# Performance work log

Hardware: AMD Instinct MI355X
Metric: run time of the kernel (lower is better)

Reference implementation:

```python
import jax, jax.numpy as jnp
import numpy as np

N_FIELDS = 8
N_NODES = 100000
N_EDGES = 6400000


def setup_inputs() -> dict:
    key = jax.random.key(0)
    k1, k2, k3, k4, k5 = jax.random.split(key, 5)
    q = jax.random.normal(k1, (N_FIELDS, N_NODES), dtype=jnp.float32)
    edges = jax.random.normal(k2, (N_EDGES, 1), dtype=jnp.float32)
    senders = jax.random.randint(k3, (N_EDGES,), 0, N_NODES, dtype=jnp.int32)
    receivers = jax.random.randint(k4, (N_EDGES,), 0, N_NODES, dtype=jnp.int32)
    dt = jax.random.uniform(k5, (1,), dtype=jnp.float32)
    # learned parameters, initialized exactly as in DeltaQGNN.__init__
    w_self = jnp.linspace(0.05, 0.09, N_FIELDS)
    w_msg = jnp.linspace(0.02, 0.04, N_FIELDS)
    w_edge = jnp.linspace(0.01, 0.03, N_FIELDS)
    b = jnp.linspace(0.005, 0.008, N_FIELDS)
    return {"q": q, "edges": edges, "senders": senders, "receivers": receivers,
            "dt": dt, "w_self": w_self, "w_msg": w_msg, "w_edge": w_edge, "b": b}


def reference(q, edges, senders, receivers, dt, w_self, w_msg, w_edge, b):
    # q: [F, N], edges: [E, 1], senders/receivers: [E], dt: [1]
    n_nodes = q.shape[1]
    edge_scalar = edges[:, 0]                                    # [E]
    # gather sender values for all fields at once: [F, E]
    msg_in = q[:, senders] + w_edge[:, None] * edge_scalar[None, :]
    # scatter-add to receivers per field: [F, N]
    msg = jax.vmap(lambda m: jax.ops.segment_sum(m, receivers, num_segments=n_nodes))(msg_in)
    rhs = w_self[:, None] * q + w_msg[:, None] * msg + b[:, None]
    return dt * rhs                                              # [F, N]
```

## Files before the change

### kernel.cpp

```cpp
#include <hip/hip_runtime.h>

#define NF 8
#define BSHIFT 8
#define BNODES 256
#define MAXNB 512
#define TPB 256
#define TPR 512
#define TPBF 512
#define CHUNKF 3072
#define KPE 6
#define NBLKF 1024
#define CAPB 17408
#define SPLIT 8
#define CAP 24
#define IDXSTR 26
#define LSLICE 2560

__global__ void k_transpose(const float* __restrict__ q, float* __restrict__ qT,
                            float* __restrict__ govf, unsigned* __restrict__ gcur,
                            int n_nodes, int nb) {
    int n = blockIdx.x * blockDim.x + threadIdx.x;
    if (n < nb) gcur[n] = 0u;
    if (n >= n_nodes) return;
    float4 a, b;
    a.x = q[0 * n_nodes + n]; a.y = q[1 * n_nodes + n];
    a.z = q[2 * n_nodes + n]; a.w = q[3 * n_nodes + n];
    b.x = q[4 * n_nodes + n]; b.y = q[5 * n_nodes + n];
    b.z = q[6 * n_nodes + n]; b.w = q[7 * n_nodes + n];
    float4* dst = reinterpret_cast<float4*>(qT + (size_t)n * NF);
    dst[0] = a; dst[1] = b;
    float* o = govf + (size_t)n * 9;
#pragma unroll
    for (int k = 0; k < 9; ++k) o[k] = 0.f;
}

__global__ __launch_bounds__(TPBF) void k_scatter_fused(
        const float* __restrict__ edges, const int* __restrict__ senders,
        const int* __restrict__ receivers, int n_edges, int nb, int tiles,
        unsigned* __restrict__ gcur, const float* __restrict__ qT,
        float* __restrict__ govf, uint2* __restrict__ rec) {
    __shared__ uint2 lrec[CHUNKF];
    __shared__ unsigned short lbkt[CHUNKF];
    __shared__ unsigned hist[MAXNB];
    __shared__ unsigned lbase[MAXNB];
    __shared__ unsigned gbase[MAXNB];

    for (int t = blockIdx.x; t < tiles; t += gridDim.x) {
        int start = t * CHUNKF;
        int end = min(start + CHUNKF, n_edges);
        int n = end - start;

        for (int i = threadIdx.x; i < nb; i += TPBF) hist[i] = 0u;
        __syncthreads();

        unsigned rcx[KPE], rcy[KPE], meta[KPE];
#pragma unroll
        for (int k = 0; k < KPE; ++k) {
            int i = (int)threadIdx.x + k * TPBF;
            meta[k] = 0xFFFFFFFFu;
            if (i < n) {
                int e = start + i;
                int s = senders[e];
                int r = receivers[e];
                float ev = edges[e];
                unsigned bkt = (unsigned)r >> BSHIFT;
                unsigned p = atomicAdd(&hist[bkt], 1u);
                rcx[k] = ((unsigned)(r & (BNODES - 1)) << 17) | (unsigned)s;
                rcy[k] = __float_as_uint(ev);
                meta[k] = (p << 9) | bkt;
            }
        }
        __syncthreads();

        if (threadIdx.x < (unsigned)nb)
            gbase[threadIdx.x] = atomicAdd(&gcur[threadIdx.x], hist[threadIdx.x]);
        if (threadIdx.x < 64) {
            int lane = threadIdx.x;
            unsigned carry = 0;
            for (int base = 0; base < nb; base += 64) {
                int bi = base + lane;
                unsigned v = (bi < nb) ? hist[bi] : 0u;
                unsigned x = v;
                for (int d = 1; d < 64; d <<= 1) {
                    unsigned y = __shfl_up(x, d, 64);
                    if (lane >= d) x += y;
                }
                if (bi < nb) lbase[bi] = carry + x - v;
                carry += __shfl(x, 63, 64);
            }
        }
        __syncthreads();

#pragma unroll
        for (int k = 0; k < KPE; ++k) {
            if (meta[k] != 0xFFFFFFFFu) {
                unsigned bkt = meta[k] & 0x1FFu;
                unsigned p   = meta[k] >> 9;
                unsigned slot = lbase[bkt] + p;
                lrec[slot] = make_uint2(rcx[k], rcy[k]);
                lbkt[slot] = (unsigned short)bkt;
            }
        }
        __syncthreads();

        for (int j = threadIdx.x; j < n; j += TPBF) {
            unsigned bkt = lbkt[j];
            uint2 rc = lrec[j];
            unsigned off = gbase[bkt] + ((unsigned)j - lbase[bkt]);
            if (off < CAPB) {
                rec[(size_t)bkt * CAPB + off] = rc;
            } else {
                unsigned snd = rc.x & 0x1FFFFu;
                unsigned rl = rc.x >> 17;
                float ev = __uint_as_float(rc.y);
                const float4* qs = reinterpret_cast<const float4*>(qT + (size_t)snd * NF);
                float4 q0 = qs[0];
                float4 q1 = qs[1];
                float* a = govf + ((size_t)bkt * BNODES + rl) * 9;
                atomicAdd(a + 0, q0.x); atomicAdd(a + 1, q0.y);
                atomicAdd(a + 2, q0.z); atomicAdd(a + 3, q0.w);
                atomicAdd(a + 4, q1.x); atomicAdd(a + 5, q1.y);
                atomicAdd(a + 6, q1.z); atomicAdd(a + 7, q1.w);
                atomicAdd(a + 8, ev);
            }
        }
        __syncthreads();
    }
}

__global__ __launch_bounds__(TPR) void k_reduce_slot(
        const uint2* __restrict__ rec, const unsigned* __restrict__ gcur,
        const float* __restrict__ qT, float* __restrict__ part,
        float* __restrict__ govf, int n_nodes) {
    __shared__ __align__(16) uint2 lrec[LSLICE];
    __shared__ unsigned short idx[BNODES * IDXSTR];
    __shared__ unsigned cur[BNODES];
    int t = threadIdx.x;
    if (t < BNODES) cur[t] = 0;

    int bkt = blockIdx.x / SPLIT;
    int s   = blockIdx.x % SPLIT;
    unsigned len = gcur[bkt];
    if (len > CAPB) len = CAPB;
    size_t base = (size_t)bkt * CAPB;
    unsigned a0 = ((unsigned)(((unsigned long long)len * s) / SPLIT)) & ~1u;
    unsigned a1 = (s + 1 == SPLIT) ? len
                : ((unsigned)(((unsigned long long)len * (s + 1)) / SPLIT)) & ~1u;
    unsigned slice = a1 - a0;
    unsigned staged = slice < LSLICE ? slice : LSLICE;

    {
        int wid = t >> 6, lane = t & 63;
        unsigned ncalls = (staged * 8u + 1023u) >> 10;
        const char* g0 = (const char*)(rec + base + a0);
        for (unsigned c = wid; c < ncalls; c += TPR / 64) {
            const char* g = g0 + (size_t)c * 1024 + (size_t)lane * 16;
            char* l = (char*)lrec + (size_t)c * 1024;
            __builtin_amdgcn_global_load_lds(
                (const __attribute__((address_space(1))) void*)g,
                (__attribute__((address_space(3))) void*)l, 16, 0, 0);
        }
    }
    __syncthreads();

    for (unsigned i = t; i < staged; i += TPR) {
        uint2 rc = lrec[i];
        unsigned rl = rc.x >> 17;
        unsigned pos = atomicAdd(&cur[rl], 1u);
        if (pos < CAP) {
            idx[rl * IDXSTR + pos] = (unsigned short)i;
        } else {
            unsigned snd = rc.x & 0x1FFFFu;
            float ev = __uint_as_float(rc.y);
            const float4* qs = reinterpret_cast<const float4*>(qT + (size_t)snd * NF);
            float4 q0 = qs[0];
            float4 q1 = qs[1];
            float* a = govf + ((size_t)bkt * BNODES + rl) * 9;
            atomicAdd(a + 0, q0.x); atomicAdd(a + 1, q0.y);
            atomicAdd(a + 2, q0.z); atomicAdd(a + 3, q0.w);
            atomicAdd(a + 4, q1.x); atomicAdd(a + 5, q1.y);
            atomicAdd(a + 6, q1.z); atomicAdd(a + 7, q1.w);
            atomicAdd(a + 8, ev);
        }
    }
    for (unsigned i = LSLICE + t; i < slice; i += TPR) {
        uint2 rc = rec[base + a0 + i];
        unsigned rl = rc.x >> 17;
        unsigned pos = atomicAdd(&cur[rl], 1u);
        if (pos < CAP) {
            idx[rl * IDXSTR + pos] = (unsigned short)i;
        } else {
            unsigned snd = rc.x & 0x1FFFFu;
            float ev = __uint_as_float(rc.y);
            const float4* qs = reinterpret_cast<const float4*>(qT + (size_t)snd * NF);
            float4 q0 = qs[0];
            float4 q1 = qs[1];
            float* a = govf + ((size_t)bkt * BNODES + rl) * 9;
            atomicAdd(a + 0, q0.x); atomicAdd(a + 1, q0.y);
            atomicAdd(a + 2, q0.z); atomicAdd(a + 3, q0.w);
            atomicAdd(a + 4, q1.x); atomicAdd(a + 5, q1.y);
            atomicAdd(a + 6, q1.z); atomicAdd(a + 7, q1.w);
            atomicAdd(a + 8, ev);
        }
    }
    __syncthreads();

    int node = t >> 1;
    int parity = t & 1;
    float m[9];
#pragma unroll
    for (int k = 0; k < 9; ++k) m[k] = 0.f;
    unsigned cntv = cur[node];
    if (cntv > CAP) cntv = CAP;
    for (unsigned j = parity; j < cntv; j += 2) {
        unsigned i0 = idx[node * IDXSTR + j];
        uint2 rc0 = (i0 < LSLICE) ? lrec[i0] : rec[base + a0 + i0];
        const float4* qs0 = reinterpret_cast<const float4*>(qT + (size_t)(rc0.x & 0x1FFFFu) * NF);
        float4 a0v = qs0[0], a1v = qs0[1];
        m[0] += a0v.x; m[1] += a0v.y; m[2] += a0v.z; m[3] += a0v.w;
        m[4] += a1v.x; m[5] += a1v.y; m[6] += a1v.z; m[7] += a1v.w;
        m[8] += __uint_as_float(rc0.y);
    }
    __syncthreads();

    float* scratch = reinterpret_cast<float*>(lrec);
    if (parity == 1) {
        float* d = scratch + (size_t)node * 9;
#pragma unroll
        for (int k = 0; k < 9; ++k) d[k] = m[k];
    }
    __syncthreads();
    if (parity == 0) {
        const float* p2 = scratch + (size_t)node * 9;
        float* dst = part + (size_t)blockIdx.x * (BNODES * 9) + (size_t)node * 9;
#pragma unroll
        for (int k = 0; k < 9; ++k) dst[k] = m[k] + p2[k];
    }
}

__global__ void k_finalize2(const float* __restrict__ part, const float* __restrict__ govf,
                            const float* __restrict__ q,
                            const float* __restrict__ dtp, const float* __restrict__ w_self,
                            const float* __restrict__ w_msg, const float* __restrict__ w_edge,
                            const float* __restrict__ bv, float* __restrict__ out,
                            int split, int n_nodes) {
    int n = blockIdx.x * blockDim.x + threadIdx.x;
    if (n >= n_nodes) return;
    int bkt = n >> BSHIFT;
    int rl = n & (BNODES - 1);
    float m[9];
#pragma unroll
    for (int f = 0; f < 9; ++f) m[f] = govf[(size_t)n * 9 + f];
    for (int s = 0; s < split; ++s) {
        const float* p = part + ((size_t)(bkt * split + s) * BNODES + rl) * 9;
#pragma unroll
        for (int f = 0; f < 9; ++f) m[f] += p[f];
    }
    float dtv = dtp[0];
    float evs = m[8];
#pragma unroll
    for (int f = 0; f < NF; ++f) {
        float msg = m[f] + w_edge[f] * evs;
        out[(size_t)f * n_nodes + n] =
            dtv * (w_self[f] * q[(size_t)f * n_nodes + n] + w_msg[f] * msg + bv[f]);
    }
}

__global__ void k_transpose_zero(const float* __restrict__ q, float* __restrict__ qT,
                                 float* __restrict__ msgT, int n_nodes) {
    int n = blockIdx.x * blockDim.x + threadIdx.x;
    if (n >= n_nodes) return;
    float v[NF];
#pragma unroll
    for (int f = 0; f < NF; ++f) v[f] = q[f * n_nodes + n];
    float4* dst = reinterpret_cast<float4*>(qT + (size_t)n * NF);
    dst[0] = make_float4(v[0], v[1], v[2], v[3]);
    dst[1] = make_float4(v[4], v[5], v[6], v[7]);
    float4 z = make_float4(0.f, 0.f, 0.f, 0.f);
    float4* m = reinterpret_cast<float4*>(msgT + (size_t)n * NF);
    m[0] = z; m[1] = z;
}

__global__ void k_edge_scatter(const float* __restrict__ edges, const int* __restrict__ senders,
                               const int* __restrict__ receivers, const float* __restrict__ qT,
                               float* __restrict__ msgT, const float* __restrict__ w_edge,
                               int n_edges) {
    float we[NF];
#pragma unroll
    for (int f = 0; f < NF; ++f) we[f] = w_edge[f];
    int idx = blockIdx.x * blockDim.x + threadIdx.x;
    int stride = gridDim.x * blockDim.x;
    for (int e = idx; e < n_edges; e += stride) {
        int s = senders[e];
        int r = receivers[e];
        float ev = edges[e];
        const float4* qs = reinterpret_cast<const float4*>(qT + (size_t)s * NF);
        float4 q0 = qs[0];
        float4 q1 = qs[1];
        float* m = msgT + (size_t)r * NF;
        atomicAdd(m + 0, q0.x + we[0] * ev);
        atomicAdd(m + 1, q0.y + we[1] * ev);
        atomicAdd(m + 2, q0.z + we[2] * ev);
        atomicAdd(m + 3, q0.w + we[3] * ev);
        atomicAdd(m + 4, q1.x + we[4] * ev);
        atomicAdd(m + 5, q1.y + we[5] * ev);
        atomicAdd(m + 6, q1.z + we[6] * ev);
        atomicAdd(m + 7, q1.w + we[7] * ev);
    }
}

__global__ void k_finalize(const float* __restrict__ q, const float* __restrict__ msgT,
                           const float* __restrict__ dt, const float* __restrict__ w_self,
                           const float* __restrict__ w_msg, const float* __restrict__ b,
                           float* __restrict__ out, int n_nodes) {
    int n = blockIdx.x * blockDim.x + threadIdx.x;
    if (n >= n_nodes) return;
    float dtv = dt[0];
    const float4* m4 = reinterpret_cast<const float4*>(msgT + (size_t)n * NF);
    float4 m0 = m4[0];
    float4 m1 = m4[1];
    float mv[NF] = {m0.x, m0.y, m0.z, m0.w, m1.x, m1.y, m1.z, m1.w};
#pragma unroll
    for (int f = 0; f < NF; ++f) {
        out[f * n_nodes + n] = dtv * (w_self[f] * q[f * n_nodes + n] + w_msg[f] * mv[f] + b[f]);
    }
}

extern "C" void kernel_launch(void* const* d_in, const int* in_sizes, int n_in,
                              void* d_out, int out_size, void* d_ws, size_t ws_size,
                              hipStream_t stream) {
    const float* q         = (const float*)d_in[0];
    const float* edges     = (const float*)d_in[1];
    const int*   senders   = (const int*)d_in[2];
    const int*   receivers = (const int*)d_in[3];
    const float* dt        = (const float*)d_in[4];
    const float* w_self    = (const float*)d_in[5];
    const float* w_msg     = (const float*)d_in[6];
    const float* w_edge    = (const float*)d_in[7];
    const float* b         = (const float*)d_in[8];
    float* out = (float*)d_out;

    const int n_nodes = in_sizes[0] / NF;
    const int n_edges = in_sizes[2];
    const int nb = (n_nodes + BNODES - 1) >> BSHIFT;
    const int tiles = (n_edges + CHUNKF - 1) / CHUNKF;

    size_t rec_bytes  = (size_t)nb * CAPB * 8;
    size_t qT_bytes   = (size_t)n_nodes * NF * 4;
    size_t gcur_bytes = 256 + (size_t)nb * 4;
    size_t govf_bytes = (size_t)nb * BNODES * 9 * 4;
    size_t part_bytes = (size_t)SPLIT * nb * BNODES * 9 * 4;
    size_t need = rec_bytes + qT_bytes + gcur_bytes + govf_bytes + part_bytes + 4096;

    double mean_per_bucket = (double)n_edges / (double)nb;
    bool ok = (n_nodes <= 131072) && (nb <= MAXNB) && (need <= ws_size) &&
              (mean_per_bucket + 8.0 * __builtin_sqrt(mean_per_bucket) < (double)CAPB);

    if (ok) {
        char* p = (char*)d_ws;
        uint2*    rec  = (uint2*)p;    p += rec_bytes;
        float*    qT   = (float*)p;    p += qT_bytes;
        unsigned* gcur = (unsigned*)p; p += gcur_bytes;
        float*    govf = (float*)p;    p += govf_bytes;
        float*    part = (float*)(((uintptr_t)p + 255) & ~(uintptr_t)255);

        int nblk_f = tiles < NBLKF ? tiles : NBLKF;

        k_transpose<<<(n_nodes + TPB - 1) / TPB, TPB, 0, stream>>>(q, qT, govf, gcur,
                                                                   n_nodes, nb);
        k_scatter_fused<<<nblk_f, TPBF, 0, stream>>>(edges, senders, receivers, n_edges,
                                                     nb, tiles, gcur, qT, govf, rec);
        k_reduce_slot<<<nb * SPLIT, TPR, 0, stream>>>(rec, gcur, qT, part, govf, n_nodes);
        k_finalize2<<<(n_nodes + TPB - 1) / TPB, TPB, 0, stream>>>(
            part, govf, q, dt, w_self, w_msg, w_edge, b, out, SPLIT, n_nodes);
    } else {
        float* qT   = (float*)d_ws;
        float* msgT = qT + (size_t)n_nodes * NF;
        k_transpose_zero<<<(n_nodes + TPB - 1) / TPB, TPB, 0, stream>>>(q, qT, msgT, n_nodes);
        k_edge_scatter<<<3072, TPB, 0, stream>>>(edges, senders, receivers, qT, msgT,
                                                 w_edge, n_edges);
        k_finalize<<<(n_nodes + TPB - 1) / TPB, TPB, 0, stream>>>(q, msgT, dt, w_self, w_msg,
                                                                  b, out, n_nodes);
    }
}
```

Before: 123.4 us.

## Fuse record staging with slot counting and enlarge fill-kernel blocks

Drops the separate async global-to-LDS staging pass and its barrier in the reduce kernel. Each thread now loads two records with one 16-byte load, writes them to shared memory and does the slot atomics right away, so the staging latency overlaps with the counting work. It also adds a barrier after zeroing the counters, which fixes a race in the old code. Separately, the fill kernel moves to 1024 threads per block with a doubled chunk and half as many blocks, which changes occupancy and per-block work. One risk: the uint4 load reads an extra 8 bytes past an odd-length slice, which is harmless only if that memory is allocated.

```diff
diff --git a/kernel.cpp b/kernel.cpp
--- a/kernel.cpp
+++ b/kernel.cpp
@@ -6,10 +6,10 @@
 #define MAXNB 512
 #define TPB 256
 #define TPR 512
-#define TPBF 512
-#define CHUNKF 3072
+#define TPBF 1024
+#define CHUNKF 6144
 #define KPE 6
-#define NBLKF 1024
+#define NBLKF 512
 #define CAPB 17408
 #define SPLIT 8
 #define CAP 24
@@ -137,6 +137,7 @@
     __shared__ unsigned cur[BNODES];
     int t = threadIdx.x;
     if (t < BNODES) cur[t] = 0;
+    __syncthreads();
 
     int bkt = blockIdx.x / SPLIT;
     int s   = blockIdx.x % SPLIT;
@@ -149,38 +150,46 @@
     unsigned slice = a1 - a0;
     unsigned staged = slice < LSLICE ? slice : LSLICE;
 
-    {
-        int wid = t >> 6, lane = t & 63;
-        unsigned ncalls = (staged * 8u + 1023u) >> 10;
-        const char* g0 = (const char*)(rec + base + a0);
-        for (unsigned c = wid; c < ncalls; c += TPR / 64) {
-            const char* g = g0 + (size_t)c * 1024 + (size_t)lane * 16;
-            char* l = (char*)lrec + (size_t)c * 1024;
-            __builtin_amdgcn_global_load_lds(
-                (const __attribute__((address_space(1))) void*)g,
-                (__attribute__((address_space(3))) void*)l, 16, 0, 0);
-        }
-    }
-    __syncthreads();
-
-    for (unsigned i = t; i < staged; i += TPR) {
-        uint2 rc = lrec[i];
-        unsigned rl = rc.x >> 17;
-        unsigned pos = atomicAdd(&cur[rl], 1u);
-        if (pos < CAP) {
-            idx[rl * IDXSTR + pos] = (unsigned short)i;
-        } else {
-            unsigned snd = rc.x & 0x1FFFFu;
-            float ev = __uint_as_float(rc.y);
-            const float4* qs = reinterpret_cast<const float4*>(qT + (size_t)snd * NF);
-            float4 q0 = qs[0];
-            float4 q1 = qs[1];
-            float* a = govf + ((size_t)bkt * BNODES + rl) * 9;
-            atomicAdd(a + 0, q0.x); atomicAdd(a + 1, q0.y);
-            atomicAdd(a + 2, q0.z); atomicAdd(a + 3, q0.w);
-            atomicAdd(a + 4, q1.x); atomicAdd(a + 5, q1.y);
-            atomicAdd(a + 6, q1.z); atomicAdd(a + 7, q1.w);
-            atomicAdd(a + 8, ev);
+    for (unsigned i = 2u * t; i < staged; i += 2u * TPR) {
+        uint4 two = *reinterpret_cast<const uint4*>(rec + base + a0 + i);
+        *reinterpret_cast<uint4*>(lrec + i) = two;
+        {
+            unsigned rl = two.x >> 17;
+            unsigned pos = atomicAdd(&cur[rl], 1u);
+            if (pos < CAP) {
+                idx[rl * IDXSTR + pos] = (unsigned short)i;
+            } else {
+                unsigned snd = two.x & 0x1FFFFu;
+                float ev = __uint_as_float(two.y);
+                const float4* qs = reinterpret_cast<const float4*>(qT + (size_t)snd * NF);
+                float4 q0 = qs[0];
+                float4 q1 = qs[1];
+                float* a = govf + ((size_t)bkt * BNODES + rl) * 9;
+                atomicAdd(a + 0, q0.x); atomicAdd(a + 1, q0.y);
+                atomicAdd(a + 2, q0.z); atomicAdd(a + 3, q0.w);
+                atomicAdd(a + 4, q1.x); atomicAdd(a + 5, q1.y);
+                atomicAdd(a + 6, q1.z); atomicAdd(a + 7, q1.w);
+                atomicAdd(a + 8, ev);
+            }
+        }
+        if (i + 1 < staged) {
+            unsigned rl = two.z >> 17;
+            unsigned pos = atomicAdd(&cur[rl], 1u);
+            if (pos < CAP) {
+                idx[rl * IDXSTR + pos] = (unsigned short)(i + 1);
+            } else {
+                unsigned snd = two.z & 0x1FFFFu;
+                float ev = __uint_as_float(two.w);
+                const float4* qs = reinterpret_cast<const float4*>(qT + (size_t)snd * NF);
+                float4 q0 = qs[0];
+                float4 q1 = qs[1];
+                float* a = govf + ((size_t)bkt * BNODES + rl) * 9;
+                atomicAdd(a + 0, q0.x); atomicAdd(a + 1, q0.y);
+                atomicAdd(a + 2, q0.z); atomicAdd(a + 3, q0.w);
+                atomicAdd(a + 4, q1.x); atomicAdd(a + 5, q1.y);
+                atomicAdd(a + 6, q1.z); atomicAdd(a + 7, q1.w);
+                atomicAdd(a + 8, ev);
+            }
         }
     }
     for (unsigned i = LSLICE + t; i < slice; i += TPR) {
```

After: 107.2 us. 13.1% less time.
